# Kernel tuning notes

Measured on AMD Instinct MI355X. Metric: run time of the kernel, lower is better.

## Reference

```python
import jax, jax.numpy as jnp
import numpy as np

D = 1280        # embed_dim
H = 20          # num heads
HD = D // H     # head_dim = 64
FFN = 5120
SEQ = 4096
NSEG = 8
EPS = 1e-5


def _ln(x, g, b):
    mu = jnp.mean(x, axis=-1, keepdims=True)
    var = jnp.var(x, axis=-1, keepdims=True)
    return (x - mu) * jax.lax.rsqrt(var + EPS) * g + b


def setup_inputs() -> dict:
    key = jax.random.key(0)
    ks = jax.random.split(key, 16)
    s = 0.02
    inp = {
        "hidden_states": jax.random.normal(ks[0], (SEQ, D), dtype=jnp.float32),
        "cu_seqlens": jnp.arange(NSEG + 1, dtype=jnp.int32) * (SEQ // NSEG),
        "Wq": jax.random.normal(ks[1], (D, D), dtype=jnp.float32) * s,
        "bq": jnp.zeros((D,), jnp.float32),
        "Wk": jax.random.normal(ks[2], (D, D), dtype=jnp.float32) * s,
        "Wv": jax.random.normal(ks[3], (D, D), dtype=jnp.float32) * s,
        "bv": jnp.zeros((D,), jnp.float32),
        "Wo": jax.random.normal(ks[4], (D, D), dtype=jnp.float32) * s,
        "bo": jnp.zeros((D,), jnp.float32),
        "ln1_g": jnp.ones((D,), jnp.float32),
        "ln1_b": jnp.zeros((D,), jnp.float32),
        "Wf1": jax.random.normal(ks[5], (D, FFN), dtype=jnp.float32) * s,
        "bf1": jnp.zeros((FFN,), jnp.float32),
        "Wf2": jax.random.normal(ks[6], (FFN, D), dtype=jnp.float32) * s,
        "bf2": jnp.zeros((D,), jnp.float32),
        "ln2_g": jnp.ones((D,), jnp.float32),
        "ln2_b": jnp.zeros((D,), jnp.float32),
    }
    return inp


def reference(hidden_states, cu_seqlens, Wq, bq, Wk, Wv, bv, Wo, bo,
              ln1_g, ln1_b, Wf1, bf1, Wf2, bf2, ln2_g, ln2_b):
    seq = hidden_states.shape[0]
    # --- self-attention block ---
    residual = hidden_states
    x = _ln(hidden_states, ln1_g, ln1_b)
    q = (x @ Wq + bq).reshape(seq, H, HD).transpose(1, 0, 2)   # [H,S,hd]
    k = (x @ Wk).reshape(seq, H, HD).transpose(1, 0, 2)
    v = (x @ Wv + bv).reshape(seq, H, HD).transpose(1, 0, 2)
    scores = jnp.einsum('hqd,hkd->hqk', q, k) / jnp.sqrt(jnp.float32(HD))
    # block-diagonal mask from cu_seqlens (segment id per token)
    pos = jnp.arange(seq, dtype=jnp.int32)
    seg = jnp.searchsorted(cu_seqlens, pos, side='right')      # [S]
    same = seg[None, :, None] == seg[None, None, :]            # [1,S,S]
    neg = jnp.finfo(scores.dtype).min
    scores = jnp.where(same, scores, scores + neg)
    attn = jax.nn.softmax(scores, axis=-1)
    attn_out = jnp.einsum('hqk,hkd->hqd', attn, v).transpose(1, 0, 2).reshape(seq, D)
    attn_out = attn_out @ Wo + bo
    h = residual + attn_out
    # --- FFN block ---
    residual = h
    y = _ln(h, ln2_g, ln2_b)
    y = jax.nn.gelu(y @ Wf1 + bf1, approximate=False)
    y = y @ Wf2 + bf2
    return residual + y
```

## Files before the change

kernel.cpp:

```cpp
#include <hip/hip_runtime.h>
#include <cstdint>
#include <cstddef>

#define SEQ_ 4096
#define DIM_ 1280
#define NHEAD_ 20
#define HDIM_ 64
#define FFN_ 5120
#define SEG_ 512
#define QKVN_ 3840

typedef __attribute__((ext_vector_type(8))) short bf16x8;
typedef __attribute__((ext_vector_type(4))) float f32x4;
typedef __attribute__((ext_vector_type(8))) unsigned short us8;
typedef __attribute__((ext_vector_type(4))) unsigned short us4;

__device__ __forceinline__ unsigned short f2b(float f) {
  unsigned int u = __builtin_bit_cast(unsigned int, f);
  u += 0x7fffu + ((u >> 16) & 1u);
  return (unsigned short)(u >> 16);
}

__device__ __forceinline__ float b2f(unsigned short u) {
  return __builtin_bit_cast(float, (unsigned int)u << 16);
}

__device__ __forceinline__ void gload_lds16(const void* g, void* l) {
  __builtin_amdgcn_global_load_lds(
      (const __attribute__((address_space(1))) unsigned int*)g,
      (__attribute__((address_space(3))) unsigned int*)l, 16, 0, 0);
}

#define WAITVM(N) asm volatile("s_waitcnt vmcnt(" #N ")" ::: "memory")

__global__ __launch_bounds__(256) void transp_ln_kernel(
    const float* __restrict__ Wq, const float* __restrict__ Wk,
    const float* __restrict__ Wv, const float* __restrict__ Wo,
    const float* __restrict__ Wf1, const float* __restrict__ Wf2,
    unsigned short* __restrict__ Wqkvt, unsigned short* __restrict__ Wot,
    unsigned short* __restrict__ Wf1t, unsigned short* __restrict__ Wf2t,
    const float* __restrict__ hidden, const float* __restrict__ g1,
    const float* __restrict__ b1, unsigned short* __restrict__ xln) {
  int t = blockIdx.x;
  if (t >= 19200) {
    int row = t - 19200, tid = threadIdx.x;
    int l = tid & 63, w = tid >> 6;
    const float* x = hidden + (size_t)row * DIM_;
    float v[5], s = 0.f, s2 = 0.f;
#pragma unroll
    for (int i = 0; i < 5; ++i) {
      v[i] = x[tid + i * 256];
      s += v[i];
      s2 += v[i] * v[i];
    }
#pragma unroll
    for (int off = 1; off < 64; off <<= 1) {
      s += __shfl_xor(s, off);
      s2 += __shfl_xor(s2, off);
    }
    __shared__ float red[8];
    if (l == 0) { red[w * 2] = s; red[w * 2 + 1] = s2; }
    __syncthreads();
    s = red[0] + red[2] + red[4] + red[6];
    s2 = red[1] + red[3] + red[5] + red[7];
    float mu = s * (1.f / DIM_);
    float var = s2 * (1.f / DIM_) - mu * mu;
    float rs = rsqrtf(var + 1e-5f);
#pragma unroll
    for (int i = 0; i < 5; ++i) {
      int c = tid + i * 256;
      xln[(size_t)row * DIM_ + c] = f2b((v[i] - mu) * rs * g1[c] + b1[c]);
    }
    return;
  }
  __shared__ float tile[32][33];
  const float* in;
  unsigned short* out;
  int R, C, bx, by;
  if (t < 6400) {
    int m = t / 1600, lt = t - m * 1600;
    in = (m == 0) ? Wq : (m == 1) ? Wk : (m == 2) ? Wv : Wo;
    out = (m < 3) ? Wqkvt + (size_t)m * DIM_ * DIM_ : Wot;
    R = DIM_; C = DIM_;
    bx = lt % 40; by = lt / 40;
  } else if (t < 12800) {
    int lt = t - 6400;
    in = Wf1; out = Wf1t; R = DIM_; C = FFN_;
    bx = lt % 160; by = lt / 160;
  } else {
    int lt = t - 12800;
    in = Wf2; out = Wf2t; R = FFN_; C = DIM_;
    bx = lt % 40; by = lt / 40;
  }
  int c0 = bx * 32, r0 = by * 32;
  int tx = threadIdx.x & 31, ty = threadIdx.x >> 5;
#pragma unroll
  for (int i = 0; i < 32; i += 8)
    tile[ty + i][tx] = in[(size_t)(r0 + ty + i) * C + c0 + tx];
  __syncthreads();
#pragma unroll
  for (int i = 0; i < 32; i += 8)
    out[(size_t)(c0 + ty + i) * R + r0 + tx] = f2b(tile[tx][ty + i]);
}

enum { EPI_QKV = 0, EPI_GELU = 3, EPI_PART = 4 };

template <int EPI>
__device__ __forceinline__ void gemm_body(
    const unsigned short* __restrict__ A, int lda,
    const unsigned short* __restrict__ Bt, int ldb,
    const float* __restrict__ bias, const float* __restrict__ bias2,
    void* __restrict__ out0, void* __restrict__ out1, void* __restrict__ out2,
    int M, int N, int K, int nz) {
  __shared__ char lds[3][24576];
  const int tid = threadIdx.x;
  const int l = tid & 63, w = tid >> 6;
  const int r16 = l & 15, kg4 = l >> 4;
  const int nx = gridDim.x;
  const int orig = blockIdx.y * nx + blockIdx.x;
  const int xcd = orig & 7, idx = orig >> 3;
  const int by = xcd * (gridDim.y >> 3) + idx / nx;
  const int bx = idx % nx;
  const int m0 = by * 128, n0 = bx * 256;
  const int wm = (w >> 2) * 64, wn = (w & 3) * 64;
  const int z = blockIdx.z;
  const int ntK = K >> 5;
  const int base = ntK / nz, rem = ntK % nz;
  const int k0 = z * base + (z < rem ? z : rem);
  const int nt = base + (z < rem ? 1 : 0);
  const int kc = (tid & 3) ^ ((tid >> 3) & 3);
  const unsigned short* aA = A + (size_t)(m0 + (tid >> 2)) * lda + kc * 8 + k0 * 32;
  const unsigned short* aB = Bt + (size_t)(n0 + (tid >> 2)) * ldb + kc * 8 + k0 * 32;
  const unsigned short* aB1 = aB + (size_t)128 * ldb;
  const int cswz = (kg4 ^ ((r16 >> 1) & 3)) << 4;
  int aoff[4], boff[4];
#pragma unroll
  for (int mi = 0; mi < 4; ++mi) aoff[mi] = (wm + mi * 16 + r16) * 64 + cswz;
#pragma unroll
  for (int ni = 0; ni < 4; ++ni) boff[ni] = 8192 + (wn + ni * 16 + r16) * 64 + cswz;

  f32x4 acc[4][4] = {};

#define STAGE(b, kt_)                                          \
  do {                                                         \
    const int kb = (kt_) * 32;                                 \
    char* dA = &lds[0][0] + (b) * 24576 + w * 1024;            \
    char* dB = dA + 8192;                                      \
    gload_lds16(aA + kb, dA);                                  \
    gload_lds16(aB + kb, dB);                                  \
    gload_lds16(aB1 + kb, dB + 8192);                          \
  } while (0)

  STAGE(0, 0);
  if (nt > 1) {
    STAGE(1, 1);
    WAITVM(3);
  } else {
    WAITVM(0);
  }
  __builtin_amdgcn_s_barrier();

  int cur = 0;
#pragma unroll 1
  for (int t = 0; t < nt; ++t) {
    if (t + 2 < nt) {
      int nxt = cur + 2; if (nxt >= 3) nxt -= 3;
      STAGE(nxt, t + 2);
    }
    const char* sl = &lds[0][0] + cur * 24576;
    bf16x8 af[4], bfv[4];
#pragma unroll
    for (int mi = 0; mi < 4; ++mi) af[mi] = *(const bf16x8*)(sl + aoff[mi]);
#pragma unroll
    for (int ni = 0; ni < 4; ++ni) bfv[ni] = *(const bf16x8*)(sl + boff[ni]);
    __builtin_amdgcn_s_setprio(1);
#pragma unroll
    for (int mi = 0; mi < 4; ++mi)
#pragma unroll
      for (int ni = 0; ni < 4; ++ni)
        acc[mi][ni] = __builtin_amdgcn_mfma_f32_16x16x32_bf16(af[mi], bfv[ni], acc[mi][ni], 0, 0, 0);
    __builtin_amdgcn_s_setprio(0);
    if (t + 2 < nt) WAITVM(3);
    else if (t + 1 < nt) WAITVM(0);
    if (t + 1 < nt) __builtin_amdgcn_s_barrier();
    ++cur; if (cur == 3) cur = 0;
  }
#undef STAGE

  const int rg = kg4 * 4;
#pragma unroll
  for (int mi = 0; mi < 4; ++mi) {
#pragma unroll
    for (int ni = 0; ni < 4; ++ni) {
      int row = m0 + wm + mi * 16 + rg;
      int col = n0 + wn + ni * 16 + r16;
      f32x4 v = acc[mi][ni];
      if constexpr (EPI == EPI_QKV) {
        if (col < DIM_) {
          unsigned short* O = (unsigned short*)out0;
          float bb = bias[col];
#pragma unroll
          for (int j = 0; j < 4; ++j) O[(size_t)(row + j) * DIM_ + col] = f2b(v[j] + bb);
        } else if (col < 2 * DIM_) {
          unsigned short* O = (unsigned short*)out1;
          int cc = col - DIM_;
#pragma unroll
          for (int j = 0; j < 4; ++j) O[(size_t)(row + j) * DIM_ + cc] = f2b(v[j]);
        } else {
          unsigned short* O = (unsigned short*)out2;
          int cc = col - 2 * DIM_;
          float bb = bias2[cc];
          us4 pk;
#pragma unroll
          for (int j = 0; j < 4; ++j) pk[j] = f2b(v[j] + bb);
          *(us4*)(O + (size_t)cc * SEQ_ + row) = pk;
        }
      } else if constexpr (EPI == EPI_GELU) {
        unsigned short* O = (unsigned short*)out0;
        float bb = bias[col];
#pragma unroll
        for (int j = 0; j < 4; ++j) {
          float t = v[j] + bb;
          t = 0.5f * t * (1.f + erff(t * 0.70710678118f));
          O[(size_t)(row + j) * N + col] = f2b(t);
        }
      } else {
        unsigned short* O = (unsigned short*)out0 + (size_t)blockIdx.z * M * N;
#pragma unroll
        for (int j = 0; j < 4; ++j) O[(size_t)(row + j) * N + col] = f2b(v[j]);
      }
    }
  }
}

__global__ __launch_bounds__(512, 4) void qkv_gemm(
    const unsigned short* A, const unsigned short* Bt, const float* bq,
    const float* bv, void* q, void* k, void* v) {
  gemm_body<EPI_QKV>(A, DIM_, Bt, DIM_, bq, bv, q, k, v, SEQ_, QKVN_, DIM_, 1);
}
__global__ __launch_bounds__(512, 4) void wo_gemm(
    const unsigned short* A, const unsigned short* Bt, void* part) {
  gemm_body<EPI_PART>(A, DIM_, Bt, DIM_, nullptr, nullptr, part, nullptr, nullptr,
                      SEQ_, DIM_, DIM_, 3);
}
__global__ __launch_bounds__(512, 4) void ffn1_gemm(
    const unsigned short* A, const unsigned short* Bt, const float* bf1, void* g) {
  gemm_body<EPI_GELU>(A, DIM_, Bt, DIM_, bf1, nullptr, g, nullptr, nullptr,
                      SEQ_, FFN_, DIM_, 1);
}
__global__ __launch_bounds__(512, 4) void ffn2_gemm(
    const unsigned short* A, const unsigned short* Bt, void* part) {
  gemm_body<EPI_PART>(A, FFN_, Bt, FFN_, nullptr, nullptr, part, nullptr, nullptr,
                      SEQ_, DIM_, FFN_, 3);
}

__global__ __launch_bounds__(256) void reduce3_kernel(
    const unsigned short* __restrict__ part, const float* __restrict__ bias,
    const float* __restrict__ res, float* __restrict__ out) {
  const size_t MN = (size_t)SEQ_ * DIM_;
  for (size_t i = blockIdx.x * 256 + threadIdx.x; i * 4 < MN; i += (size_t)gridDim.x * 256) {
    size_t e = i * 4;
    us4 a = *(const us4*)(part + e);
    us4 b = *(const us4*)(part + MN + e);
    us4 c = *(const us4*)(part + 2 * MN + e);
    f32x4 r = *(const f32x4*)(res + e);
    f32x4 bb = *(const f32x4*)(bias + (int)(e % DIM_));
    f32x4 o;
#pragma unroll
    for (int j = 0; j < 4; ++j) o[j] = b2f(a[j]) + b2f(b[j]) + b2f(c[j]) + r[j] + bb[j];
    *(f32x4*)(out + e) = o;
  }
}

__global__ __launch_bounds__(256) void reduce3_ln_kernel(
    const unsigned short* __restrict__ part, const float* __restrict__ bias,
    const float* __restrict__ res, const float* __restrict__ g,
    const float* __restrict__ b, float* __restrict__ hout,
    unsigned short* __restrict__ yout) {
  const size_t MN = (size_t)SEQ_ * DIM_;
  int row = blockIdx.x, tid = threadIdx.x;
  int l = tid & 63, w = tid >> 6;
  float v[5], s = 0.f, s2 = 0.f;
#pragma unroll
  for (int i = 0; i < 5; ++i) {
    int c = tid + i * 256;
    size_t e = (size_t)row * DIM_ + c;
    float t = b2f(part[e]) + b2f(part[MN + e]) + b2f(part[2 * MN + e]) + bias[c] + res[e];
    hout[e] = t;
    v[i] = t;
    s += t;
    s2 += t * t;
  }
#pragma unroll
  for (int off = 1; off < 64; off <<= 1) {
    s += __shfl_xor(s, off);
    s2 += __shfl_xor(s2, off);
  }
  __shared__ float red[8];
  if (l == 0) { red[w * 2] = s; red[w * 2 + 1] = s2; }
  __syncthreads();
  s = red[0] + red[2] + red[4] + red[6];
  s2 = red[1] + red[3] + red[5] + red[7];
  float mu = s * (1.f / DIM_);
  float var = s2 * (1.f / DIM_) - mu * mu;
  float rs = rsqrtf(var + 1e-5f);
#pragma unroll
  for (int i = 0; i < 5; ++i) {
    int c = tid + i * 256;
    yout[(size_t)row * DIM_ + c] = f2b((v[i] - mu) * rs * g[c] + b[c]);
  }
}

__global__ __launch_bounds__(256) void attn_kernel(
    const unsigned short* __restrict__ Q, const unsigned short* __restrict__ Kb,
    const unsigned short* __restrict__ Vt, unsigned short* __restrict__ O) {
  __shared__ unsigned short S[64][512];
  int tid = threadIdx.x;
  int l = tid & 63, w = tid >> 6;
  int orig = blockIdx.x;
  int b = (orig & 7) * (gridDim.x >> 3) + (orig >> 3);
  int qc = b & 7, seg = (b >> 3) & 7, hh = b >> 6;
  int r16 = l & 15, kg = l >> 4, rg = (l >> 4) * 4;
  int qrow0 = seg * SEG_ + qc * 64 + w * 16;
  bf16x8 aq[2];
#pragma unroll
  for (int ks = 0; ks < 2; ++ks)
    aq[ks] = *(const bf16x8*)(Q + (size_t)(qrow0 + r16) * DIM_ + hh * HDIM_ + ks * 32 + kg * 8);
#pragma unroll 4
  for (int kc = 0; kc < 32; ++kc) {
    f32x4 acc = {};
    __builtin_amdgcn_s_setprio(1);
#pragma unroll
    for (int ks = 0; ks < 2; ++ks) {
      bf16x8 bk = *(const bf16x8*)(Kb + (size_t)(seg * SEG_ + kc * 16 + r16) * DIM_ +
                                   hh * HDIM_ + ks * 32 + kg * 8);
      acc = __builtin_amdgcn_mfma_f32_16x16x32_bf16(aq[ks], bk, acc, 0, 0, 0);
    }
    __builtin_amdgcn_s_setprio(0);
#pragma unroll
    for (int j = 0; j < 4; ++j)
      S[w * 16 + rg + j][kc * 16 + r16] = f2b(acc[j] * 0.125f);
  }
#pragma unroll 2
  for (int r = 0; r < 16; ++r) {
    unsigned short* Sr = &S[w * 16 + r][0];
    us8 raw = *(const us8*)(Sr + l * 8);
    float ev[8];
#pragma unroll
    for (int j = 0; j < 8; ++j) ev[j] = b2f(raw[j]);
    float m = fmaxf(fmaxf(fmaxf(ev[0], ev[1]), fmaxf(ev[2], ev[3])),
                    fmaxf(fmaxf(ev[4], ev[5]), fmaxf(ev[6], ev[7])));
#pragma unroll
    for (int off = 1; off < 64; off <<= 1) m = fmaxf(m, __shfl_xor(m, off));
    float sum = 0.f;
#pragma unroll
    for (int j = 0; j < 8; ++j) { ev[j] = __expf(ev[j] - m); sum += ev[j]; }
#pragma unroll
    for (int off = 1; off < 64; off <<= 1) sum += __shfl_xor(sum, off);
    float inv = 1.f / sum;
    us8 pk;
#pragma unroll
    for (int j = 0; j < 8; ++j) pk[j] = f2b(ev[j] * inv);
    *(us8*)(Sr + ((l ^ (r & 7)) * 8)) = pk;
  }
  f32x4 oacc[4] = {};
  const unsigned short* Pr = &S[w * 16 + r16][0];
  int rowx = r16 & 7;
#pragma unroll 2
  for (int ks = 0; ks < 16; ++ks) {
    int chunk = (ks * 4 + kg) ^ rowx;
    bf16x8 pa = *(const bf16x8*)(Pr + chunk * 8);
    __builtin_amdgcn_s_setprio(1);
#pragma unroll
    for (int df = 0; df < 4; ++df) {
      bf16x8 bv = *(const bf16x8*)(Vt + (size_t)(hh * HDIM_ + df * 16 + r16) * SEQ_ +
                                   seg * SEG_ + ks * 32 + kg * 8);
      oacc[df] = __builtin_amdgcn_mfma_f32_16x16x32_bf16(pa, bv, oacc[df], 0, 0, 0);
    }
    __builtin_amdgcn_s_setprio(0);
  }
#pragma unroll
  for (int df = 0; df < 4; ++df)
#pragma unroll
    for (int j = 0; j < 4; ++j)
      O[(size_t)(qrow0 + rg + j) * DIM_ + hh * HDIM_ + df * 16 + r16] = f2b(oacc[df][j]);
}

extern "C" void kernel_launch(void* const* d_in, const int* in_sizes, int n_in,
                              void* d_out, int out_size, void* d_ws, size_t ws_size,
                              hipStream_t stream) {
  (void)in_sizes; (void)n_in; (void)out_size; (void)ws_size;
  const float* hidden = (const float*)d_in[0];
  const float* Wq = (const float*)d_in[2];
  const float* bq = (const float*)d_in[3];
  const float* Wk = (const float*)d_in[4];
  const float* Wv = (const float*)d_in[5];
  const float* bv = (const float*)d_in[6];
  const float* Wo = (const float*)d_in[7];
  const float* bo = (const float*)d_in[8];
  const float* g1 = (const float*)d_in[9];
  const float* b1 = (const float*)d_in[10];
  const float* Wf1 = (const float*)d_in[11];
  const float* bf1 = (const float*)d_in[12];
  const float* Wf2 = (const float*)d_in[13];
  const float* bf2 = (const float*)d_in[14];
  const float* g2 = (const float*)d_in[15];
  const float* b2 = (const float*)d_in[16];

  char* p = (char*)d_ws;
  auto alloc = [&](size_t bytes) {
    char* r = p;
    p += (bytes + 255) & ~(size_t)255;
    return r;
  };
  unsigned short* xln   = (unsigned short*)alloc((size_t)SEQ_ * DIM_ * 2);
  unsigned short* Wqkvt = (unsigned short*)alloc((size_t)DIM_ * QKVN_ * 2);
  unsigned short* Wot   = (unsigned short*)alloc((size_t)DIM_ * DIM_ * 2);
  unsigned short* Wf1t  = (unsigned short*)alloc((size_t)DIM_ * FFN_ * 2);
  unsigned short* Wf2t  = (unsigned short*)alloc((size_t)DIM_ * FFN_ * 2);
  unsigned short* Qb    = (unsigned short*)alloc((size_t)SEQ_ * DIM_ * 2);
  unsigned short* Kbf   = (unsigned short*)alloc((size_t)SEQ_ * DIM_ * 2);
  unsigned short* Vtb   = (unsigned short*)alloc((size_t)SEQ_ * DIM_ * 2);
  unsigned short* attnb = (unsigned short*)alloc((size_t)SEQ_ * DIM_ * 2);
  float*          hbuf  = (float*)alloc((size_t)SEQ_ * DIM_ * 4);
  unsigned short* ybuf  = (unsigned short*)alloc((size_t)SEQ_ * DIM_ * 2);
  unsigned short* gbuf  = (unsigned short*)alloc((size_t)SEQ_ * FFN_ * 2);
  unsigned short* part3 = (unsigned short*)alloc((size_t)3 * SEQ_ * DIM_ * 2);

  transp_ln_kernel<<<19200 + SEQ_, 256, 0, stream>>>(
      Wq, Wk, Wv, Wo, Wf1, Wf2, Wqkvt, Wot, Wf1t, Wf2t, hidden, g1, b1, xln);
  qkv_gemm<<<dim3(QKVN_ / 256, SEQ_ / 128), 512, 0, stream>>>(
      xln, Wqkvt, bq, bv, Qb, Kbf, Vtb);
  attn_kernel<<<NHEAD_ * 8 * 8, 256, 0, stream>>>(Qb, Kbf, Vtb, attnb);
  wo_gemm<<<dim3(DIM_ / 256, SEQ_ / 128, 3), 512, 0, stream>>>(attnb, Wot, part3);
  reduce3_ln_kernel<<<SEQ_, 256, 0, stream>>>(part3, bo, hidden, g2, b2, hbuf, ybuf);
  ffn1_gemm<<<dim3(FFN_ / 256, SEQ_ / 128), 512, 0, stream>>>(ybuf, Wf1t, bf1, gbuf);
  ffn2_gemm<<<dim3(DIM_ / 256, SEQ_ / 128, 3), 512, 0, stream>>>(gbuf, Wf2t, part3);
  reduce3_kernel<<<2048, 256, 0, stream>>>(part3, bf2, hbuf, (float*)d_out);
}
```

Before: 367.7 us.

## Stage K and V tiles in LDS with swizzled async loads for attention

The attention kernel now cooperatively loads 128-key chunks of K and V into a swizzled shared-memory buffer using direct global-to-LDS loads, and the MFMA operands are read from LDS. Before, each wave fetched the same K/V data straight from global memory. The intent is to cut redundant global traffic across the four waves and to get coalesced loads. The cost is an extra 16KB of LDS, which may lower occupancy, plus barriers and full waits each chunk with no double buffering.

Result: faster. 318.6 us (-13.4%).

```diff
diff --git a/kernel.cpp b/kernel.cpp
--- a/kernel.cpp
+++ b/kernel.cpp
@@ -315,6 +315,7 @@
     const unsigned short* __restrict__ Q, const unsigned short* __restrict__ Kb,
     const unsigned short* __restrict__ Vt, unsigned short* __restrict__ O) {
   __shared__ unsigned short S[64][512];
+  __shared__ unsigned short KV[8192];
   int tid = threadIdx.x;
   int l = tid & 63, w = tid >> 6;
   int orig = blockIdx.x;
@@ -326,20 +327,36 @@
 #pragma unroll
   for (int ks = 0; ks < 2; ++ks)
     aq[ks] = *(const bf16x8*)(Q + (size_t)(qrow0 + r16) * DIM_ + hh * HDIM_ + ks * 32 + kg * 8);
-#pragma unroll 4
-  for (int kc = 0; kc < 32; ++kc) {
-    f32x4 acc = {};
-    __builtin_amdgcn_s_setprio(1);
-#pragma unroll
-    for (int ks = 0; ks < 2; ++ks) {
-      bf16x8 bk = *(const bf16x8*)(Kb + (size_t)(seg * SEG_ + kc * 16 + r16) * DIM_ +
-                                   hh * HDIM_ + ks * 32 + kg * 8);
-      acc = __builtin_amdgcn_mfma_f32_16x16x32_bf16(aq[ks], bk, acc, 0, 0, 0);
-    }
-    __builtin_amdgcn_s_setprio(0);
-#pragma unroll
-    for (int j = 0; j < 4; ++j)
-      S[w * 16 + rg + j][kc * 16 + r16] = f2b(acc[j] * 0.125f);
+#pragma unroll 1
+  for (int kcc = 0; kcc < 4; ++kcc) {
+    __syncthreads();
+#pragma unroll
+    for (int i = 0; i < 4; ++i) {
+      int slot = i * 256 + tid;
+      int r = slot >> 3, cp = slot & 7;
+      int kc = cp ^ (r & 7);
+      gload_lds16(Kb + (size_t)(seg * SEG_ + kcc * 128 + r) * DIM_ + hh * HDIM_ + kc * 8,
+                  (char*)KV + slot * 16);
+    }
+    WAITVM(0);
+    __syncthreads();
+#pragma unroll
+    for (int kcl = 0; kcl < 8; ++kcl) {
+      f32x4 acc = {};
+      __builtin_amdgcn_s_setprio(1);
+#pragma unroll
+      for (int ks = 0; ks < 2; ++ks) {
+        int c = ks * 4 + kg;
+        bf16x8 bk = *(const bf16x8*)((const char*)KV +
+                      ((kcl * 16 + r16) * 8 + (c ^ (r16 & 7))) * 16);
+        acc = __builtin_amdgcn_mfma_f32_16x16x32_bf16(aq[ks], bk, acc, 0, 0, 0);
+      }
+      __builtin_amdgcn_s_setprio(0);
+      int kcg = kcc * 8 + kcl;
+#pragma unroll
+      for (int j = 0; j < 4; ++j)
+        S[w * 16 + rg + j][kcg * 16 + r16] = f2b(acc[j] * 0.125f);
+    }
   }
 #pragma unroll 2
   for (int r = 0; r < 16; ++r) {
@@ -366,18 +383,35 @@
   f32x4 oacc[4] = {};
   const unsigned short* Pr = &S[w * 16 + r16][0];
   int rowx = r16 & 7;
-#pragma unroll 2
-  for (int ks = 0; ks < 16; ++ks) {
-    int chunk = (ks * 4 + kg) ^ rowx;
-    bf16x8 pa = *(const bf16x8*)(Pr + chunk * 8);
-    __builtin_amdgcn_s_setprio(1);
-#pragma unroll
-    for (int df = 0; df < 4; ++df) {
-      bf16x8 bv = *(const bf16x8*)(Vt + (size_t)(hh * HDIM_ + df * 16 + r16) * SEQ_ +
-                                   seg * SEG_ + ks * 32 + kg * 8);
-      oacc[df] = __builtin_amdgcn_mfma_f32_16x16x32_bf16(pa, bv, oacc[df], 0, 0, 0);
-    }
-    __builtin_amdgcn_s_setprio(0);
+#pragma unroll 1
+  for (int vcc = 0; vcc < 4; ++vcc) {
+    __syncthreads();
+#pragma unroll
+    for (int i = 0; i < 4; ++i) {
+      int slot = i * 256 + tid;
+      int r = slot >> 4, cp = slot & 15;
+      int kc = (cp & 8) | ((cp & 7) ^ (r & 7));
+      gload_lds16(Vt + (size_t)(hh * HDIM_ + r) * SEQ_ + seg * SEG_ + vcc * 128 + kc * 8,
+                  (char*)KV + slot * 16);
+    }
+    WAITVM(0);
+    __syncthreads();
+#pragma unroll
+    for (int ksl = 0; ksl < 4; ++ksl) {
+      int ks = vcc * 4 + ksl;
+      int chunk = (ks * 4 + kg) ^ rowx;
+      bf16x8 pa = *(const bf16x8*)(Pr + chunk * 8);
+      __builtin_amdgcn_s_setprio(1);
+#pragma unroll
+      for (int df = 0; df < 4; ++df) {
+        int vr = df * 16 + r16;
+        int c = ksl * 4 + kg;
+        int cp = (c & 8) | ((c & 7) ^ (vr & 7));
+        bf16x8 bv = *(const bf16x8*)((const char*)KV + (vr * 16 + cp) * 16);
+        oacc[df] = __builtin_amdgcn_mfma_f32_16x16x32_bf16(pa, bv, oacc[df], 0, 0, 0);
+      }
+      __builtin_amdgcn_s_setprio(0);
+    }
   }
 #pragma unroll
   for (int df = 0; df < 4; ++df)
```
